# Kernel optimization log

Hardware: AMD Instinct MI355X
Metric: run time of the kernel (lower is better)

Reference implementation:

```python
import jax, jax.numpy as jnp
import numpy as np

EPS = 1e-8  # torch.nn.CosineSimilarity eps


def setup_inputs() -> dict:
    key = jax.random.key(0)
    k1, k2, k3 = jax.random.split(key, 3)
    C, S, D = 1024, 16, 512
    x = jax.random.normal(k1, (C, S, D), dtype=jnp.float32)
    w = jax.random.normal(k2, (1,), dtype=jnp.float32)
    b = jax.random.normal(k3, (1,), dtype=jnp.float32)
    return {"x": x, "w": w, "b": b}


def reference(x, w, b):
    # stable_ge2e: leave-one-out positive centroids, full negative centroids.
    C, S, D = x.shape
    wp = jax.nn.softplus(w)  # (1,)

    sum_c = x.sum(axis=1)                      # (C, D)
    mean_c = sum_c / S                         # negative centroids (C, D)
    loo = (sum_c[:, None, :] - x) / (S - 1.0)  # leave-one-out centroids (C, S, D)

    nx = jnp.linalg.norm(x, axis=-1)           # (C, S)
    nmean = jnp.linalg.norm(mean_c, axis=-1)   # (C,)
    nloo = jnp.linalg.norm(loo, axis=-1)       # (C, S)

    # cosine similarities (clamped denominator, as in torch CosineSimilarity)
    sim_neg = jnp.einsum('jid,kd->jik', x, mean_c) / jnp.maximum(
        nx[:, :, None] * nmean[None, None, :], EPS)          # (C, S, C)
    sim_pos = jnp.einsum('jid,jid->ji', x, loo) / jnp.maximum(nx * nloo, EPS)  # (C, S)

    # on the diagonal k == j use the leave-one-out positive centroid
    eye = jnp.eye(C, dtype=bool)
    sim = jnp.where(eye[:, None, :], sim_pos[:, :, None], sim_neg)  # (C, S, C)

    logits = wp * sim + b
    logS = jax.nn.log_softmax(logits, axis=-1)
    Sji_j = jnp.einsum('jij->ji', logS)                        # (C, S) diagonal
    Sji_k = jax.scipy.special.logsumexp(logS, axis=-1)         # (C, S) (== 0 post-softmax)
    loss = -(Sji_j - Sji_k).reshape(-1)
    return loss.mean()
```

## Files before the change

kernel.cpp:

```cpp
#include <hip/hip_runtime.h>
#include <math.h>

#define CC 1024
#define SS 16
#define DD 512
#define RR (CC*SS)
#define EPSV 1e-8f
#define LDB 520

typedef __attribute__((ext_vector_type(8))) short short8;
typedef __attribute__((ext_vector_type(4))) float f32x4;
typedef unsigned short ushort_t;

__device__ __forceinline__ unsigned short f2bf(float f) {
  unsigned u = __float_as_uint(f);
  u += 0x7fffu + ((u >> 16) & 1u);
  return (unsigned short)(u >> 16);
}

__device__ __forceinline__ void async16(void* l, const void* g) {
  __builtin_amdgcn_global_load_lds(
      (const __attribute__((address_space(1))) void*)g,
      (__attribute__((address_space(3))) void*)l, 16, 0, 0);
}

__device__ __forceinline__ float softplusf(float v) {
  return (v > 20.f) ? v : log1pf(expf(v));
}

__global__ __launch_bounds__(256) void k_pre(
    const float* __restrict__ x, unsigned* __restrict__ mn,
    float* __restrict__ nx, float* __restrict__ simpos,
    ushort_t* __restrict__ xn) {
  __shared__ float xs[SS * DD];
  __shared__ float sums[DD];
  __shared__ float red[4];
  __shared__ float snm;
  __shared__ float rinv[SS];
  const int j = blockIdx.x, tid = threadIdx.x;
  const float4* xj = (const float4*)(x + (size_t)j * SS * DD);
  float4* xs4 = (float4*)xs;
  for (int i = tid; i < SS * DD / 4; i += 256) xs4[i] = xj[i];
  __syncthreads();
  float m2 = 0.f;
  {
    const int d0 = tid * 2;
    float s0 = 0.f, s1 = 0.f;
#pragma unroll
    for (int i = 0; i < SS; ++i) {
      s0 += xs[i * DD + d0];
      s1 += xs[i * DD + d0 + 1];
    }
    sums[d0] = s0; sums[d0 + 1] = s1;
    float ma = s0 * (1.0f / SS), mb = s1 * (1.0f / SS);
    m2 = fmaf(ma, ma, mb * mb);
  }
#pragma unroll
  for (int off = 32; off > 0; off >>= 1) m2 += __shfl_xor(m2, off, 64);
  const int wid = tid >> 6, lane = tid & 63;
  if (lane == 0) red[wid] = m2;
  __syncthreads();
  if (tid == 0) snm = sqrtf(red[0] + red[1] + red[2] + red[3]);
  __syncthreads();
  const float inm = (1.0f / SS) / snm;
  {
    const int d0 = tid * 2;
    unsigned lo = f2bf(sums[d0] * inm);
    unsigned hi = f2bf(sums[d0 + 1] * inm);
    mn[((size_t)j * DD + d0) >> 1] = lo | (hi << 16);
  }
  for (int i = wid; i < SS; i += 4) {
    float nx2 = 0.f, dxs = 0.f, t2 = 0.f;
    for (int d = lane; d < DD; d += 64) {
      float xv = xs[i * DD + d];
      float sc = sums[d];
      nx2 = fmaf(xv, xv, nx2);
      dxs = fmaf(xv, sc, dxs);
      float tv = sc - xv;
      t2 = fmaf(tv, tv, t2);
    }
#pragma unroll
    for (int off = 32; off > 0; off >>= 1) {
      nx2 += __shfl_xor(nx2, off, 64);
      dxs += __shfl_xor(dxs, off, 64);
      t2  += __shfl_xor(t2,  off, 64);
    }
    if (lane == 0) {
      float nxv = sqrtf(nx2);
      float tn  = sqrtf(t2);
      float num = (dxs - nx2) * (1.0f / (SS - 1));
      float den = fmaxf(nxv * tn * (1.0f / (SS - 1)), EPSV);
      nx[j * SS + i] = nxv;
      rinv[i] = 1.0f / nxv;
      simpos[j * SS + i] = num / den;
    }
  }
  __syncthreads();
  if (xn) {
    uint2* dst = (uint2*)(xn + (size_t)j * SS * DD);
    for (int idx = tid; idx < SS * DD / 4; idx += 256) {
      const int e = idx * 4;
      const float ri = rinv[e >> 9];
      unsigned a = f2bf(xs[e] * ri),     b2 = f2bf(xs[e + 1] * ri);
      unsigned c = f2bf(xs[e + 2] * ri), d2 = f2bf(xs[e + 3] * ri);
      dst[idx] = make_uint2(a | (b2 << 16), c | (d2 << 16));
    }
  }
}

template <bool USE_XN>
__global__ __launch_bounds__(256, 2) void k_gemm(
    const float* __restrict__ x, const ushort_t* __restrict__ xn,
    const ushort_t* __restrict__ mn, const float* __restrict__ nx,
    const float* __restrict__ simpos, const float* __restrict__ wptr,
    const float* __restrict__ bptr, float* __restrict__ ps) {
  __shared__ ushort_t bs[2][32 * LDB];
  const int tid = threadIdx.x;
  const int wid = tid >> 6, lane = tid & 63;
  const int cL = lane & 15, quad = lane >> 4;
  const int rb = (int)blockIdx.x >> 2, cb = (int)blockIdx.x & 3;
  const int r0 = rb * 128, cbase = cb * 256;
  const float wp = softplusf(wptr[0]), bv = bptr[0];

  short8 af[2][16];
  int jw[2];
  float sp[2][4], sacc[2][4];
#pragma unroll
  for (int rt = 0; rt < 2; ++rt) {
    const int row = r0 + wid * 32 + rt * 16 + cL;
    if (USE_XN) {
      const short8* src = (const short8*)(xn + (size_t)row * DD);
#pragma unroll
      for (int kc = 0; kc < 16; ++kc) af[rt][kc] = src[kc * 4 + quad];
    } else {
      const float* xr = x + (size_t)row * DD;
      const float invn = 1.0f / nx[row];
#pragma unroll
      for (int kc = 0; kc < 16; ++kc) {
        const int k0 = kc * 32 + quad * 8;
        float4 p = *(const float4*)(xr + k0);
        float4 q = *(const float4*)(xr + k0 + 4);
        short8 v;
        v[0] = f2bf(p.x * invn); v[1] = f2bf(p.y * invn);
        v[2] = f2bf(p.z * invn); v[3] = f2bf(p.w * invn);
        v[4] = f2bf(q.x * invn); v[5] = f2bf(q.y * invn);
        v[6] = f2bf(q.z * invn); v[7] = f2bf(q.w * invn);
        af[rt][kc] = v;
      }
    }
    jw[rt] = (r0 + wid * 32 + rt * 16) >> 4;
#pragma unroll
    for (int r = 0; r < 4; ++r) {
      sp[rt][r] = simpos[r0 + wid * 32 + rt * 16 + quad * 4 + r];
      sacc[rt][r] = 0.f;
    }
  }

  {
    const ushort_t* gsrc = mn + (size_t)cbase * DD;
#pragma unroll
    for (int t = 0; t < 8; ++t) {
      const int rr = wid + t * 4;
      async16(&bs[0][rr * LDB + lane * 8], gsrc + (size_t)rr * DD + lane * 8);
    }
  }
  __syncthreads();

  for (int cc = 0; cc < 8; ++cc) {
    if (cc < 7) {
      const ushort_t* gsrc = mn + (size_t)(cbase + (cc + 1) * 32) * DD;
      ushort_t* dst = bs[(cc + 1) & 1];
#pragma unroll
      for (int t = 0; t < 8; ++t) {
        const int rr = wid + t * 4;
        async16(&dst[rr * LDB + lane * 8], gsrc + (size_t)rr * DD + lane * 8);
      }
    }
    const ushort_t* B = bs[cc & 1];
    f32x4 acc[2][2];
#pragma unroll
    for (int rt = 0; rt < 2; ++rt)
#pragma unroll
      for (int f = 0; f < 2; ++f) acc[rt][f] = (f32x4){0.f, 0.f, 0.f, 0.f};
#pragma unroll
    for (int kc = 0; kc < 16; ++kc) {
      short8 bfr[2];
#pragma unroll
      for (int f = 0; f < 2; ++f)
        bfr[f] = *(const short8*)&B[(f * 16 + cL) * LDB + kc * 32 + quad * 8];
#pragma unroll
      for (int rt = 0; rt < 2; ++rt)
#pragma unroll
        for (int f = 0; f < 2; ++f)
          acc[rt][f] = __builtin_amdgcn_mfma_f32_16x16x32_bf16(
              af[rt][kc], bfr[f], acc[rt][f], 0, 0, 0);
    }
    const int c0 = cbase + cc * 32;
#pragma unroll
    for (int rt = 0; rt < 2; ++rt)
#pragma unroll
      for (int f = 0; f < 2; ++f) {
        const int cg = c0 + f * 16 + cL;
        const bool diag = (cg == jw[rt]);
#pragma unroll
        for (int r = 0; r < 4; ++r) {
          const float sim = diag ? sp[rt][r] : acc[rt][f][r];
          sacc[rt][r] += __expf(fmaf(wp, sim, bv));
        }
      }
    __syncthreads();
  }

#pragma unroll
  for (int rt = 0; rt < 2; ++rt)
#pragma unroll
    for (int r = 0; r < 4; ++r) {
      float v = sacc[rt][r];
#pragma unroll
      for (int off = 1; off < 16; off <<= 1) v += __shfl_xor(v, off, 64);
      if (cL == 0)
        ps[(size_t)(r0 + wid * 32 + rt * 16 + quad * 4 + r) * 4 + cb] = v;
    }
}

__global__ __launch_bounds__(256) void k_combine(
    const float* __restrict__ ps, const float* __restrict__ simpos,
    const float* __restrict__ wptr, const float* __restrict__ bptr,
    float* __restrict__ p2) {
  __shared__ float red[4];
  const int tid = threadIdx.x;
  const int row = blockIdx.x * 256 + tid;
  const float wp = softplusf(wptr[0]), bv = bptr[0];
  const float4 s4 = *(const float4*)(ps + (size_t)row * 4);
  const float s = (s4.x + s4.y) + (s4.z + s4.w);
  float v = logf(s) - fmaf(wp, simpos[row], bv);
#pragma unroll
  for (int off = 32; off > 0; off >>= 1) v += __shfl_xor(v, off, 64);
  if ((tid & 63) == 0) red[tid >> 6] = v;
  __syncthreads();
  if (tid == 0) p2[blockIdx.x] = red[0] + red[1] + red[2] + red[3];
}

__global__ __launch_bounds__(64) void k_fin(const float* __restrict__ p2,
                                            float* __restrict__ out) {
  const int tid = threadIdx.x;
  float v = p2[tid];
#pragma unroll
  for (int off = 32; off > 0; off >>= 1) v += __shfl_xor(v, off, 64);
  if (tid == 0) out[0] = v * (1.0f / RR);
}

extern "C" void kernel_launch(void* const* d_in, const int* in_sizes, int n_in,
                              void* d_out, int out_size, void* d_ws, size_t ws_size,
                              hipStream_t stream) {
  const float* x = (const float*)d_in[0];
  const float* w = (const float*)d_in[1];
  const float* b = (const float*)d_in[2];
  float* out = (float*)d_out;

  const size_t xn_bytes = (size_t)RR * DD * 2;
  const size_t rest = (size_t)CC * DD * 2 + (size_t)RR * 4 * 2 +
                      (size_t)RR * 4 * 4 + 64 * 4;
  const bool use_xn = ws_size >= xn_bytes + rest + 256;

  char* base = (char*)d_ws;
  ushort_t* xn = use_xn ? (ushort_t*)base : nullptr;
  char* p = base + (use_xn ? xn_bytes : 0);
  ushort_t* mn = (ushort_t*)p;  p += (size_t)CC * DD * 2;
  float* nx     = (float*)p;    p += (size_t)RR * 4;
  float* simpos = (float*)p;    p += (size_t)RR * 4;
  float* ps     = (float*)p;    p += (size_t)RR * 4 * 4;
  float* p2     = (float*)p;

  k_pre<<<CC, 256, 0, stream>>>(x, (unsigned*)mn, nx, simpos, xn);
  if (use_xn)
    k_gemm<true><<<512, 256, 0, stream>>>(x, xn, mn, nx, simpos, w, b, ps);
  else
    k_gemm<false><<<512, 256, 0, stream>>>(x, xn, mn, nx, simpos, w, b, ps);
  k_combine<<<RR / 256, 256, 0, stream>>>(ps, simpos, w, b, p2);
  k_fin<<<1, 64, 0, stream>>>(p2, out);
}
```

Baseline: 115.0 us.

## Drop LDS staging in GEMM, load centroid tiles directly from global

The GEMM kernel no longer stages centroid tiles into double-buffered LDS with async global-to-LDS loads and barriers. Each wave now reads its B fragments straight from global memory in 16-column steps, relying on L2/L1 since the centroid matrix is small. Block indexing is remapped so consecutive blocks share a column slice, and the fp32 fallback path and the nx buffer are removed so bf16 normalized rows are always used. This removes the barrier and LDS costs but adds redundant global loads per wave and assumes the workspace is always large enough.

```diff
diff --git a/kernel.cpp b/kernel.cpp
--- a/kernel.cpp
+++ b/kernel.cpp
@@ -6,7 +6,6 @@
 #define DD 512
 #define RR (CC*SS)
 #define EPSV 1e-8f
-#define LDB 520
 
 typedef __attribute__((ext_vector_type(8))) short short8;
 typedef __attribute__((ext_vector_type(4))) float f32x4;
@@ -18,20 +17,13 @@
   return (unsigned short)(u >> 16);
 }
 
-__device__ __forceinline__ void async16(void* l, const void* g) {
-  __builtin_amdgcn_global_load_lds(
-      (const __attribute__((address_space(1))) void*)g,
-      (__attribute__((address_space(3))) void*)l, 16, 0, 0);
-}
-
 __device__ __forceinline__ float softplusf(float v) {
   return (v > 20.f) ? v : log1pf(expf(v));
 }
 
 __global__ __launch_bounds__(256) void k_pre(
     const float* __restrict__ x, unsigned* __restrict__ mn,
-    float* __restrict__ nx, float* __restrict__ simpos,
-    ushort_t* __restrict__ xn) {
+    float* __restrict__ simpos, ushort_t* __restrict__ xn) {
   __shared__ float xs[SS * DD];
   __shared__ float sums[DD];
   __shared__ float red[4];
@@ -90,13 +82,12 @@
       float tn  = sqrtf(t2);
       float num = (dxs - nx2) * (1.0f / (SS - 1));
       float den = fmaxf(nxv * tn * (1.0f / (SS - 1)), EPSV);
-      nx[j * SS + i] = nxv;
       rinv[i] = 1.0f / nxv;
       simpos[j * SS + i] = num / den;
     }
   }
   __syncthreads();
-  if (xn) {
+  {
     uint2* dst = (uint2*)(xn + (size_t)j * SS * DD);
     for (int idx = tid; idx < SS * DD / 4; idx += 256) {
       const int e = idx * 4;
@@ -108,18 +99,17 @@
   }
 }
 
-template <bool USE_XN>
 __global__ __launch_bounds__(256, 2) void k_gemm(
-    const float* __restrict__ x, const ushort_t* __restrict__ xn,
-    const ushort_t* __restrict__ mn, const float* __restrict__ nx,
+    const ushort_t* __restrict__ xn, const ushort_t* __restrict__ mn,
     const float* __restrict__ simpos, const float* __restrict__ wptr,
     const float* __restrict__ bptr, float* __restrict__ ps) {
-  __shared__ ushort_t bs[2][32 * LDB];
   const int tid = threadIdx.x;
   const int wid = tid >> 6, lane = tid & 63;
   const int cL = lane & 15, quad = lane >> 4;
-  const int rb = (int)blockIdx.x >> 2, cb = (int)blockIdx.x & 3;
-  const int r0 = rb * 128, cbase = cb * 256;
+  const int bid = blockIdx.x;
+  const int rb = bid & 127, cb = bid >> 7;
+  const int r0 = rb * 128 + wid * 32;
+  const int cbase = cb * 256;
   const float wp = softplusf(wptr[0]), bv = bptr[0];
 
   short8 af[2][16];
@@ -127,88 +117,36 @@
   float sp[2][4], sacc[2][4];
 #pragma unroll
   for (int rt = 0; rt < 2; ++rt) {
-    const int row = r0 + wid * 32 + rt * 16 + cL;
-    if (USE_XN) {
-      const short8* src = (const short8*)(xn + (size_t)row * DD);
-#pragma unroll
-      for (int kc = 0; kc < 16; ++kc) af[rt][kc] = src[kc * 4 + quad];
-    } else {
-      const float* xr = x + (size_t)row * DD;
-      const float invn = 1.0f / nx[row];
-#pragma unroll
-      for (int kc = 0; kc < 16; ++kc) {
-        const int k0 = kc * 32 + quad * 8;
-        float4 p = *(const float4*)(xr + k0);
-        float4 q = *(const float4*)(xr + k0 + 4);
-        short8 v;
-        v[0] = f2bf(p.x * invn); v[1] = f2bf(p.y * invn);
-        v[2] = f2bf(p.z * invn); v[3] = f2bf(p.w * invn);
-        v[4] = f2bf(q.x * invn); v[5] = f2bf(q.y * invn);
-        v[6] = f2bf(q.z * invn); v[7] = f2bf(q.w * invn);
-        af[rt][kc] = v;
-      }
-    }
-    jw[rt] = (r0 + wid * 32 + rt * 16) >> 4;
+    const int row = r0 + rt * 16 + cL;
+    const short8* src = (const short8*)(xn + (size_t)row * DD);
+#pragma unroll
+    for (int kc = 0; kc < 16; ++kc) af[rt][kc] = src[kc * 4 + quad];
+    jw[rt] = (r0 + rt * 16) >> 4;
 #pragma unroll
     for (int r = 0; r < 4; ++r) {
-      sp[rt][r] = simpos[r0 + wid * 32 + rt * 16 + quad * 4 + r];
+      sp[rt][r] = simpos[r0 + rt * 16 + quad * 4 + r];
       sacc[rt][r] = 0.f;
     }
   }
 
-  {
-    const ushort_t* gsrc = mn + (size_t)cbase * DD;
-#pragma unroll
-    for (int t = 0; t < 8; ++t) {
-      const int rr = wid + t * 4;
-      async16(&bs[0][rr * LDB + lane * 8], gsrc + (size_t)rr * DD + lane * 8);
-    }
-  }
-  __syncthreads();
-
-  for (int cc = 0; cc < 8; ++cc) {
-    if (cc < 7) {
-      const ushort_t* gsrc = mn + (size_t)(cbase + (cc + 1) * 32) * DD;
-      ushort_t* dst = bs[(cc + 1) & 1];
-#pragma unroll
-      for (int t = 0; t < 8; ++t) {
-        const int rr = wid + t * 4;
-        async16(&dst[rr * LDB + lane * 8], gsrc + (size_t)rr * DD + lane * 8);
-      }
-    }
-    const ushort_t* B = bs[cc & 1];
-    f32x4 acc[2][2];
-#pragma unroll
-    for (int rt = 0; rt < 2; ++rt)
-#pragma unroll
-      for (int f = 0; f < 2; ++f) acc[rt][f] = (f32x4){0.f, 0.f, 0.f, 0.f};
+  for (int t = 0; t < 16; ++t) {
+    const int c0 = cbase + t * 16;
+    const ushort_t* bsrc = mn + (size_t)(c0 + cL) * DD + quad * 8;
+    f32x4 a0 = {0.f, 0.f, 0.f, 0.f}, a1 = {0.f, 0.f, 0.f, 0.f};
 #pragma unroll
     for (int kc = 0; kc < 16; ++kc) {
-      short8 bfr[2];
-#pragma unroll
-      for (int f = 0; f < 2; ++f)
-        bfr[f] = *(const short8*)&B[(f * 16 + cL) * LDB + kc * 32 + quad * 8];
-#pragma unroll
-      for (int rt = 0; rt < 2; ++rt)
-#pragma unroll
-        for (int f = 0; f < 2; ++f)
-          acc[rt][f] = __builtin_amdgcn_mfma_f32_16x16x32_bf16(
-              af[rt][kc], bfr[f], acc[rt][f], 0, 0, 0);
-    }
-    const int c0 = cbase + cc * 32;
-#pragma unroll
-    for (int rt = 0; rt < 2; ++rt)
-#pragma unroll
-      for (int f = 0; f < 2; ++f) {
-        const int cg = c0 + f * 16 + cL;
-        const bool diag = (cg == jw[rt]);
-#pragma unroll
-        for (int r = 0; r < 4; ++r) {
-          const float sim = diag ? sp[rt][r] : acc[rt][f][r];
-          sacc[rt][r] += __expf(fmaf(wp, sim, bv));
-        }
-      }
-    __syncthreads();
+      const short8 bfr = *(const short8*)(bsrc + kc * 32);
+      a0 = __builtin_amdgcn_mfma_f32_16x16x32_bf16(af[0][kc], bfr, a0, 0, 0, 0);
+      a1 = __builtin_amdgcn_mfma_f32_16x16x32_bf16(af[1][kc], bfr, a1, 0, 0, 0);
+    }
+    const bool d0 = (c0 + cL == jw[0]), d1 = (c0 + cL == jw[1]);
+#pragma unroll
+    for (int r = 0; r < 4; ++r) {
+      const float s0 = d0 ? sp[0][r] : a0[r];
+      const float s1 = d1 ? sp[1][r] : a1[r];
+      sacc[0][r] += __expf(fmaf(wp, s0, bv));
+      sacc[1][r] += __expf(fmaf(wp, s1, bv));
+    }
   }
 
 #pragma unroll
@@ -219,7 +157,7 @@
 #pragma unroll
       for (int off = 1; off < 16; off <<= 1) v += __shfl_xor(v, off, 64);
       if (cL == 0)
-        ps[(size_t)(r0 + wid * 32 + rt * 16 + quad * 4 + r) * 4 + cb] = v;
+        ps[(size_t)(r0 + rt * 16 + quad * 4 + r) * 4 + cb] = v;
     }
 }
 
@@ -258,25 +196,15 @@
   const float* b = (const float*)d_in[2];
   float* out = (float*)d_out;
 
-  const size_t xn_bytes = (size_t)RR * DD * 2;
-  const size_t rest = (size_t)CC * DD * 2 + (size_t)RR * 4 * 2 +
-                      (size_t)RR * 4 * 4 + 64 * 4;
-  const bool use_xn = ws_size >= xn_bytes + rest + 256;
-
-  char* base = (char*)d_ws;
-  ushort_t* xn = use_xn ? (ushort_t*)base : nullptr;
-  char* p = base + (use_xn ? xn_bytes : 0);
-  ushort_t* mn = (ushort_t*)p;  p += (size_t)CC * DD * 2;
-  float* nx     = (float*)p;    p += (size_t)RR * 4;
-  float* simpos = (float*)p;    p += (size_t)RR * 4;
-  float* ps     = (float*)p;    p += (size_t)RR * 4 * 4;
+  char* p = (char*)d_ws;
+  ushort_t* xn  = (ushort_t*)p;  p += (size_t)RR * DD * 2;
+  ushort_t* mn  = (ushort_t*)p;  p += (size_t)CC * DD * 2;
+  float* simpos = (float*)p;     p += (size_t)RR * 4;
+  float* ps     = (float*)p;     p += (size_t)RR * 4 * 4;
   float* p2     = (float*)p;
 
-  k_pre<<<CC, 256, 0, stream>>>(x, (unsigned*)mn, nx, simpos, xn);
-  if (use_xn)
-    k_gemm<true><<<512, 256, 0, stream>>>(x, xn, mn, nx, simpos, w, b, ps);
-  else
-    k_gemm<false><<<512, 256, 0, stream>>>(x, xn, mn, nx, simpos, w, b, ps);
+  k_pre<<<CC, 256, 0, stream>>>(x, (unsigned*)mn, simpos, xn);
+  k_gemm<<<512, 256, 0, stream>>>(xn, mn, simpos, w, b, ps);
   k_combine<<<RR / 256, 256, 0, stream>>>(ps, simpos, w, b, p2);
   k_fin<<<1, 64, 0, stream>>>(p2, out);
 }
```

Result: slower. 152.7 us (+32.8%).
